# Performance work log

Measured on AMD Instinct MI355X. Metric: run time of the kernel, lower is better.

Reference implementation:

```python
import jax, jax.numpy as jnp
import numpy as np

BASE_WEIGHT = 0.01
ADAPTATION_RATE = 0.1
EPS = 1e-8
N = 16384
H = 64


def setup_inputs() -> dict:
    key = jax.random.key(0)
    k1, k2, k3, k4 = jax.random.split(key, 4)
    return {
        "x_input": jax.random.normal(k1, (N,), dtype=jnp.float32),
        "targets": jax.random.normal(k2, (N,), dtype=jnp.float32),
        "w1": jax.random.normal(k3, (H,), dtype=jnp.float32) * 0.5,
        "b1": jnp.zeros((H,), dtype=jnp.float32),
        "w2": jax.random.normal(k4, (H,), dtype=jnp.float32) * 0.5,
        "b2": jnp.zeros((1,), dtype=jnp.float32),
    }


def _mlp(x, w1, b1, w2, b2):
    # elementwise 1 -> H -> 1 tanh MLP: predictions y_i = f(x_i)
    h = jnp.tanh(x[:, None] * w1 + b1)  # [N, H]
    return h @ w2 + b2[0]               # [N]


def _local_density(x):
    # NxN pairwise abs-diff matrix, top-3 smallest per row
    diff = jnp.abs(x[:, None] - x[None, :]) + EPS       # [N, N]
    neg_knn, _ = jax.lax.top_k(-diff, 3)                # smallest 3 via negation
    knn = -neg_knn                                       # [N, 3]
    dens = 1.0 / (knn.mean(axis=1, keepdims=True) + EPS)  # [N, 1]
    return dens / (dens.max() + EPS)


def reference(x_input, targets, w1, b1, w2, b2):
    f_sum = lambda xx: jnp.sum(_mlp(xx, w1, b1, w2, b2))
    predictions = _mlp(x_input, w1, b1, w2, b2)
    mse_loss = jnp.mean((predictions - targets) ** 2)

    # torch.autograd.grad(..., grad_outputs=ones) twice == grad of summed output twice
    dy_dx_sum = lambda xx: jnp.sum(jax.grad(f_sum)(xx))
    d2y_dx2 = jax.grad(dy_dx_sum)(x_input)               # [N]

    density = _local_density(x_input)                    # [N, 1]
    adaptive_weights = 1.0 + ADAPTATION_RATE * density   # [N, 1]
    # torch broadcasts [N,1]*[N] -> [N,N]; mean of that outer product equals
    # mean(weights) * mean(d2**2) exactly, so compute it without the NxN alloc.
    curvature_penalty = BASE_WEIGHT * (jnp.mean(adaptive_weights) * jnp.mean(d2y_dx2 ** 2))

    total_loss = mse_loss + curvature_penalty
    return (total_loss, mse_loss, curvature_penalty)
```

## Files before the change

kernel.cpp:

```cpp
#include <hip/hip_runtime.h>
#include <math.h>

#define NPTS 16384
#define HDIM 64
#define JCH 32
#define CHUNK (NPTS / JCH)
#define IBLK 256
#define NIB (NPTS / IBLK)
#define EPSF 1e-8f
#define FMAX3 3.402823466e38f

__device__ __forceinline__ void ins2(float& m1, float& m2, float d) {
    m2 = __builtin_amdgcn_fmed3f(d, m1, m2);
    m1 = fminf(d, m1);
}

__global__ __launch_bounds__(IBLK) void knn2_kernel(
    const float* __restrict__ x, float2* __restrict__ part) {
    const int jc = blockIdx.x & (JCH - 1);
    const int ic = blockIdx.x >> 5;
    const int i = ic * IBLK + threadIdx.x;
    const float xi = x[i];
    const float* __restrict__ xc = x + jc * CHUNK;

    float m1 = FMAX3, m2 = FMAX3;
    if (jc == (ic >> 1)) {
        float m3 = FMAX3;
#pragma unroll 16
        for (int k = 0; k < CHUNK; ++k) {
            float d = fabsf(xi - xc[k]);
            m3 = __builtin_amdgcn_fmed3f(d, m2, m3);
            m2 = __builtin_amdgcn_fmed3f(d, m1, m2);
            m1 = fminf(d, m1);
        }
        m1 = m2;
        m2 = m3;
    } else {
#pragma unroll 16
        for (int k = 0; k < CHUNK; ++k) {
            float d = fabsf(xi - xc[k]);
            ins2(m1, m2, d);
        }
    }
    part[jc * NPTS + i] = make_float2(m1, m2);
}

__global__ __launch_bounds__(64) void merge_kernel(
    const float* __restrict__ x, const float* __restrict__ tg,
    const float* __restrict__ w1, const float* __restrict__ b1,
    const float* __restrict__ w2, const float* __restrict__ b2,
    const float2* __restrict__ part, float* __restrict__ acc,
    float* __restrict__ out) {
    const int t = threadIdx.x;
    const int i = blockIdx.x * 64 + t;

    float m1 = FMAX3, m2 = FMAX3;
#pragma unroll
    for (int jc = 0; jc < JCH; ++jc) {
        float2 p = part[jc * NPTS + i];
        ins2(m1, m2, p.x);
        ins2(m1, m2, p.y);
    }
    float dens = 1.0f / ((m1 + m2) * (1.0f / 3.0f) + 2.0f * EPSF);

    const float xi = x[i];
    float y = b2[0];
    float d2a = 0.0f;
#pragma unroll 8
    for (int j = 0; j < HDIM; ++j) {
        float a1 = w1[j], bb = b1[j], a2 = w2[j];
        float u = fmaf(xi, a1, bb);
        float e = __expf(2.0f * u);
        float r = __builtin_amdgcn_rcpf(e + 1.0f);
        float tt = fmaf(-2.0f, r, 1.0f);
        y = fmaf(a2, tt, y);
        float g = 2.0f * tt * fmaf(tt, tt, -1.0f);
        d2a = fmaf(a2 * a1 * a1, g, d2a);
    }
    float diff = y - tg[i];
    float rs_mse = diff * diff;
    float rs_d2 = d2a * d2a;
    float rs_dn = dens, rmx = dens;
    for (int o = 32; o > 0; o >>= 1) {
        rs_mse += __shfl_down(rs_mse, o);
        rs_d2 += __shfl_down(rs_d2, o);
        rs_dn += __shfl_down(rs_dn, o);
        rmx = fmaxf(rmx, __shfl_down(rmx, o));
    }
    if (t == 0) {
        atomicAdd(&acc[0], rs_mse);
        atomicAdd(&acc[1], rs_d2);
        atomicAdd(&acc[2], rs_dn);
        atomicMax((unsigned int*)&acc[3], __float_as_uint(rmx));
        __threadfence();
        unsigned int ticket = atomicAdd((unsigned int*)&acc[4], 1u);
        if (ticket == (NPTS / 64) - 1) {
            float s_mse = atomicAdd(&acc[0], 0.0f);
            float s_d2 = atomicAdd(&acc[1], 0.0f);
            float s_dn = atomicAdd(&acc[2], 0.0f);
            float dmax = __uint_as_float(atomicMax((unsigned int*)&acc[3], 0u));
            float mse = s_mse * (1.0f / NPTS);
            float md2 = s_d2 * (1.0f / NPTS);
            float mean_density = (s_dn * (1.0f / NPTS)) / (dmax + EPSF);
            float penalty = 0.01f * (1.0f + 0.1f * mean_density) * md2;
            out[0] = mse + penalty;
            out[1] = mse;
            out[2] = penalty;
        }
    }
}

extern "C" void kernel_launch(void* const* d_in, const int* in_sizes, int n_in,
                              void* d_out, int out_size, void* d_ws, size_t ws_size,
                              hipStream_t stream) {
    const float* x = (const float*)d_in[0];
    const float* tg = (const float*)d_in[1];
    const float* w1 = (const float*)d_in[2];
    const float* b1 = (const float*)d_in[3];
    const float* w2 = (const float*)d_in[4];
    const float* b2 = (const float*)d_in[5];
    float* out = (float*)d_out;
    float* wsf = (float*)d_ws;
    float2* part = (float2*)wsf;
    float* acc = wsf + 2 * JCH * NPTS;

    hipMemsetAsync(acc, 0, 8 * sizeof(float), stream);
    hipLaunchKernelGGL(knn2_kernel, dim3(NIB * JCH), dim3(IBLK), 0, stream, x, part);
    hipLaunchKernelGGL(merge_kernel, dim3(NPTS / 64), dim3(64), 0, stream,
                       x, tg, w1, b1, w2, b2, part, acc, out);
}
```

Before: 106.5 us.

## Fuse knn and merge kernels via per-row-block last-arriver ticket

Merges the partial top-2 kNN kernel and the merge/MLP/reduction kernel into one launch. The last block to finish each row chunk, detected through a per-chunk atomic ticket, does the merge, MLP and block reduction. Per-block partial sums go to slots that a final last block sums, replacing many global float atomics. This removes one kernel launch and the gap between kernels, and cuts atomic contention. In exchange it adds fences, a ticket atomic in every block, and a serial tail run by the last block of each chunk.

```diff
diff --git a/kernel.cpp b/kernel.cpp
--- a/kernel.cpp
+++ b/kernel.cpp
@@ -15,11 +15,17 @@
     m1 = fminf(d, m1);
 }
 
-__global__ __launch_bounds__(IBLK) void knn2_kernel(
-    const float* __restrict__ x, float2* __restrict__ part) {
+__global__ __launch_bounds__(IBLK, 8) void fused_kernel(
+    const float* __restrict__ x, const float* __restrict__ tg,
+    const float* __restrict__ w1, const float* __restrict__ b1,
+    const float* __restrict__ w2, const float* __restrict__ b2,
+    float2* __restrict__ part, unsigned int* __restrict__ gticket,
+    unsigned int* __restrict__ fticket, float4* __restrict__ slot,
+    float* __restrict__ out) {
     const int jc = blockIdx.x & (JCH - 1);
     const int ic = blockIdx.x >> 5;
-    const int i = ic * IBLK + threadIdx.x;
+    const int t = threadIdx.x;
+    const int i = ic * IBLK + t;
     const float xi = x[i];
     const float* __restrict__ xc = x + jc * CHUNK;
 
@@ -43,30 +49,27 @@
         }
     }
     part[jc * NPTS + i] = make_float2(m1, m2);
-}
 
-__global__ __launch_bounds__(64) void merge_kernel(
-    const float* __restrict__ x, const float* __restrict__ tg,
-    const float* __restrict__ w1, const float* __restrict__ b1,
-    const float* __restrict__ w2, const float* __restrict__ b2,
-    const float2* __restrict__ part, float* __restrict__ acc,
-    float* __restrict__ out) {
-    const int t = threadIdx.x;
-    const int i = blockIdx.x * 64 + t;
+    __shared__ unsigned int s_tick;
+    __threadfence();
+    __syncthreads();
+    if (t == 0) s_tick = atomicAdd(&gticket[ic], 1u);
+    __syncthreads();
+    if (s_tick != JCH - 1) return;
 
-    float m1 = FMAX3, m2 = FMAX3;
+    __threadfence();
+    float M1 = FMAX3, M2 = FMAX3;
 #pragma unroll
-    for (int jc = 0; jc < JCH; ++jc) {
-        float2 p = part[jc * NPTS + i];
-        ins2(m1, m2, p.x);
-        ins2(m1, m2, p.y);
+    for (int jj = 0; jj < JCH; ++jj) {
+        float2 p = part[jj * NPTS + i];
+        ins2(M1, M2, p.x);
+        ins2(M1, M2, p.y);
     }
-    float dens = 1.0f / ((m1 + m2) * (1.0f / 3.0f) + 2.0f * EPSF);
+    float dens = 1.0f / ((M1 + M2) * (1.0f / 3.0f) + 2.0f * EPSF);
 
-    const float xi = x[i];
     float y = b2[0];
     float d2a = 0.0f;
-#pragma unroll 8
+#pragma unroll 4
     for (int j = 0; j < HDIM; ++j) {
         float a1 = w1[j], bb = b1[j], a2 = w2[j];
         float u = fmaf(xi, a1, bb);
@@ -87,21 +90,37 @@
         rs_dn += __shfl_down(rs_dn, o);
         rmx = fmaxf(rmx, __shfl_down(rmx, o));
     }
+    __shared__ float red[4][4];
+    const int wv = t >> 6, ln = t & 63;
+    if (ln == 0) {
+        red[0][wv] = rs_mse;
+        red[1][wv] = rs_d2;
+        red[2][wv] = rs_dn;
+        red[3][wv] = rmx;
+    }
+    __syncthreads();
     if (t == 0) {
-        atomicAdd(&acc[0], rs_mse);
-        atomicAdd(&acc[1], rs_d2);
-        atomicAdd(&acc[2], rs_dn);
-        atomicMax((unsigned int*)&acc[3], __float_as_uint(rmx));
+        float a0 = red[0][0] + red[0][1] + red[0][2] + red[0][3];
+        float a1 = red[1][0] + red[1][1] + red[1][2] + red[1][3];
+        float a2 = red[2][0] + red[2][1] + red[2][2] + red[2][3];
+        float am = fmaxf(fmaxf(red[3][0], red[3][1]), fmaxf(red[3][2], red[3][3]));
+        slot[ic] = make_float4(a0, a1, a2, am);
         __threadfence();
-        unsigned int ticket = atomicAdd((unsigned int*)&acc[4], 1u);
-        if (ticket == (NPTS / 64) - 1) {
-            float s_mse = atomicAdd(&acc[0], 0.0f);
-            float s_d2 = atomicAdd(&acc[1], 0.0f);
-            float s_dn = atomicAdd(&acc[2], 0.0f);
-            float dmax = __uint_as_float(atomicMax((unsigned int*)&acc[3], 0u));
-            float mse = s_mse * (1.0f / NPTS);
-            float md2 = s_d2 * (1.0f / NPTS);
-            float mean_density = (s_dn * (1.0f / NPTS)) / (dmax + EPSF);
+        unsigned int ft = atomicAdd(fticket, 1u);
+        if (ft == NIB - 1) {
+            __threadfence();
+            float s0 = 0.0f, s1 = 0.0f, s2 = 0.0f, mx = 0.0f;
+#pragma unroll 8
+            for (int g = 0; g < NIB; ++g) {
+                float4 v = slot[g];
+                s0 += v.x;
+                s1 += v.y;
+                s2 += v.z;
+                mx = fmaxf(mx, v.w);
+            }
+            float mse = s0 * (1.0f / NPTS);
+            float md2 = s1 * (1.0f / NPTS);
+            float mean_density = (s2 * (1.0f / NPTS)) / (mx + EPSF);
             float penalty = 0.01f * (1.0f + 0.1f * mean_density) * md2;
             out[0] = mse + penalty;
             out[1] = mse;
@@ -121,11 +140,13 @@
     const float* b2 = (const float*)d_in[5];
     float* out = (float*)d_out;
     float* wsf = (float*)d_ws;
+
     float2* part = (float2*)wsf;
-    float* acc = wsf + 2 * JCH * NPTS;
+    unsigned int* gticket = (unsigned int*)(wsf + 2 * JCH * NPTS);
+    unsigned int* fticket = gticket + NIB;
+    float4* slot = (float4*)(gticket + NIB + 4);
 
-    hipMemsetAsync(acc, 0, 8 * sizeof(float), stream);
-    hipLaunchKernelGGL(knn2_kernel, dim3(NIB * JCH), dim3(IBLK), 0, stream, x, part);
-    hipLaunchKernelGGL(merge_kernel, dim3(NPTS / 64), dim3(64), 0, stream,
-                       x, tg, w1, b1, w2, b2, part, acc, out);
+    hipMemsetAsync(gticket, 0, (NIB + 4) * sizeof(unsigned int), stream);
+    hipLaunchKernelGGL(fused_kernel, dim3(NIB * JCH), dim3(IBLK), 0, stream,
+                       x, tg, w1, b1, w2, b2, part, gticket, fticket, slot, out);
 }
```

After: 255.5 us. 2.4x slower.
